# Performance work log

Hardware: AMD Instinct MI355X
Metric: run time of the kernel (lower is better)

Reference implementation:

```python
import jax, jax.numpy as jnp
import numpy as np

N_NODES = 100000
DIM = 128
N_REL = 8
N_EDGES = 640000
LAMDA = 1  # indexes into [x, z1, z2]


def setup_inputs() -> dict:
    key = jax.random.key(0)
    ks = jax.random.split(key, 6)
    x = jax.random.normal(ks[0], (N_NODES, DIM), dtype=jnp.float32)
    edge_index = jax.random.randint(ks[1], (2, N_EDGES), 0, N_NODES, dtype=jnp.int32)
    edge_type = jax.random.randint(ks[2], (N_EDGES,), 0, N_REL, dtype=jnp.int32)
    edge_weight = jax.random.uniform(ks[3], (N_EDGES,), dtype=jnp.float32)
    # xavier_uniform for [R, in, out] weight stacks (fan_in=DIM, fan_out=DIM)
    limit = float(np.sqrt(6.0 / (DIM + DIM)))
    W1 = jax.random.uniform(ks[4], (N_REL, DIM, DIM), jnp.float32, -limit, limit)
    W2 = jax.random.uniform(ks[5], (N_REL, DIM, DIM), jnp.float32, -limit, limit)
    b1 = jnp.zeros((DIM,), jnp.float32)
    b2 = jnp.zeros((DIM,), jnp.float32)
    return {"x": x, "edge_index": edge_index, "edge_type": edge_type,
            "edge_weight": edge_weight, "W1": W1, "b1": b1, "W2": W2, "b2": b2}


def _ecge_conv(x, W, b, row, col, edge_type, coef, n_nodes):
    # Faithful to: msg_e = norm_e * w_e * (x[row_e] @ W[type_e]); out = scatter_add(msg, col) + b
    # Efficient form: transform every node by every relation once (N,R,D), then gather per edge.
    xW = jnp.einsum('ni,rio->nro', x, W)          # [N, R, D]
    msg = xW[row, edge_type] * coef[:, None]       # [E, D]
    out = jax.ops.segment_sum(msg, col, num_segments=n_nodes)
    return out + b


def reference(x, edge_index, edge_type, edge_weight, W1, b1, W2, b2):
    n_nodes = x.shape[0]
    row, col = edge_index[0], edge_index[1]
    # symmetric degree normalization based on destination (col) degree
    deg = jax.ops.segment_sum(jnp.ones_like(edge_weight), col, num_segments=n_nodes)
    deg_inv_sqrt = jnp.where(deg > 0, deg ** -0.5, 0.0)
    norm = deg_inv_sqrt[row] * deg_inv_sqrt[col]
    coef = norm * edge_weight

    z1 = jax.nn.relu(_ecge_conv(x, W1, b1, row, col, edge_type, coef, n_nodes))
    # F.dropout with training=False (eval mode) is identity
    z2 = _ecge_conv(z1, W2, b2, row, col, edge_type, coef, n_nodes)

    z_star = (x + z1 + z2) / 4.0
    temp = [x, z1, z2]
    z_sharp = temp[LAMDA]
    for i in range(LAMDA + 1, 3):
        z_sharp = z_sharp + temp[i]
    z_sharp = z_sharp / (4.0 - LAMDA)
    return (z_star, z_sharp)
```

## Files before the change

### kernel.cpp

```cpp
#include <hip/hip_runtime.h>
#include <hip/hip_bf16.h>
#include <cstdint>
#include <cstddef>

#define DIM  128
#define NREL 8
#define SCB  4096
#define CPB  16

typedef __attribute__((ext_vector_type(8))) short short8;
typedef __attribute__((ext_vector_type(4))) float f32x4;

static inline int cdiv(int a, int b){ return (a + b - 1) / b; }

__device__ inline unsigned short f2bf(float f){
    union { float f; uint32_t u; } v; v.f = f;
    uint32_t u = v.u;
    uint32_t r = (u + 0x7FFFu + ((u >> 16) & 1u)) >> 16;
    return (unsigned short)r;
}
__device__ inline uint32_t pack2(float lo, float hi){
    return (uint32_t)f2bf(lo) | ((uint32_t)f2bf(hi) << 16);
}
__device__ inline float bf2f(uint32_t lo16){
    union { uint32_t u; float f; } v; v.u = lo16 << 16; return v.f;
}
__device__ inline float asf(int u){
    union { int i; float f; } v; v.i = u; return v.f;
}

__global__ __launch_bounds__(256) void k_prep(const float4* __restrict__ x, unsigned short* __restrict__ xb, int n4,
                                              const int* __restrict__ col, const int* __restrict__ et, int E,
                                              int* __restrict__ cnt8, int nb4, int eb,
                                              const float* __restrict__ W1, const float* __restrict__ W2,
                                              unsigned short* __restrict__ wpk){
    int blk = blockIdx.x;
    if (blk < nb4){
        int i = blk * 256 + threadIdx.x;
        if (i >= n4) return;
        float4 v = x[i];
        ushort4 o; o.x = f2bf(v.x); o.y = f2bf(v.y); o.z = f2bf(v.z); o.w = f2bf(v.w);
        *(ushort4*)(xb + (size_t)i * 4) = o;
    } else if (blk < nb4 + eb){
        int e = (blk - nb4) * 256 + threadIdx.x;
        if (e < E) atomicAdd(&cnt8[col[e] * NREL + et[e]], 1);
    } else {
        int b = (blk - nb4 - eb) * 4 + (threadIdx.x >> 6);
        int lane = threadIdx.x & 63;
        int ks = b & 3, nt = (b >> 2) & 7, slot = b >> 5;
        const float* Wsrc = (slot < 8) ? (W1 + (size_t)slot * DIM * DIM)
                                       : (W2 + (size_t)(slot - 8) * DIM * DIM);
        int k0 = ks * 32 + (lane >> 4) * 8;
        int n  = nt * 16 + (lane & 15);
        unsigned short o[8];
        #pragma unroll
        for (int j = 0; j < 8; ++j) o[j] = f2bf(Wsrc[(size_t)(k0 + j) * DIM + n]);
        unsigned short* dst = wpk + ((size_t)b * 64 + lane) * 8;
        #pragma unroll
        for (int j = 0; j < 8; ++j) dst[j] = o[j];
    }
}

__global__ __launch_bounds__(256) void k_colsum(const int* __restrict__ cnt8, int N, int* __restrict__ colCnt){
    int c = blockIdx.x * 256 + threadIdx.x;
    if (c >= N) return;
    int s = 0;
    #pragma unroll
    for (int t = 0; t < NREL; ++t) s += cnt8[c * NREL + t];
    colCnt[c] = s;
}

__global__ __launch_bounds__(256) void k_scan1(const int* __restrict__ cnt, int M, int* __restrict__ bsum){
    int t = threadIdx.x;
    int base = blockIdx.x * SCB + t * 16;
    int s = 0;
    #pragma unroll
    for (int k = 0; k < 16; ++k){
        int i = base + k;
        if (i < M) s += cnt[i];
    }
    #pragma unroll
    for (int o = 1; o < 64; o <<= 1) s += __shfl_xor(s, o);
    __shared__ int wsum[4];
    if ((t & 63) == 0) wsum[t >> 6] = s;
    __syncthreads();
    if (t == 0) bsum[blockIdx.x] = wsum[0] + wsum[1] + wsum[2] + wsum[3];
}

__global__ void k_scan2(int* __restrict__ bsum, int NBS, int* __restrict__ total){
    if (threadIdx.x == 0){
        int a = 0;
        for (int i = 0; i < NBS; ++i){ int v = bsum[i]; bsum[i] = a; a += v; }
        *total = a;
    }
}

__global__ __launch_bounds__(256) void k_scan3(const int* __restrict__ cnt, int M,
                                               const int* __restrict__ bsum, const int* __restrict__ total,
                                               int* __restrict__ startArr, int* __restrict__ pos){
    int t = threadIdx.x;
    int base = blockIdx.x * SCB + t * 16;
    int vals[16];
    int s = 0;
    #pragma unroll
    for (int k = 0; k < 16; ++k){
        int i = base + k;
        vals[k] = (i < M) ? cnt[i] : 0;
        s += vals[k];
    }
    int lane = t & 63, w = t >> 6;
    int v = s;
    #pragma unroll
    for (int o = 1; o < 64; o <<= 1){
        int u = __shfl_up(v, o);
        if (lane >= o) v += u;
    }
    __shared__ int wsum[4];
    if (lane == 63) wsum[w] = v;
    __syncthreads();
    int excl = v - s + bsum[blockIdx.x];
    for (int i = 0; i < w; ++i) excl += wsum[i];
    #pragma unroll
    for (int k = 0; k < 16; ++k){
        int i = base + k;
        if (i < M){ startArr[i] = excl; pos[i] = excl; excl += vals[k]; }
    }
    if (blockIdx.x == 0 && t == 0) startArr[M] = *total;
}

__global__ __launch_bounds__(256) void k_place(const int* __restrict__ row, const int* __restrict__ col,
                                               const int* __restrict__ et, const float* __restrict__ ew,
                                               const int* __restrict__ colCnt,
                                               int E, int* __restrict__ pos8, int2* __restrict__ pkm){
    int e = blockIdx.x * 256 + threadIdx.x;
    if (e >= E) return;
    int r = row[e], c = col[e], t = et[e];
    int dr = colCnt[r], dc = colCnt[c];
    float a = dr > 0 ? rsqrtf((float)dr) : 0.f;
    float b = dc > 0 ? rsqrtf((float)dc) : 0.f;
    float cf = a * b * ew[e];
    int p = atomicAdd(&pos8[c * NREL + t], 1);
    union { float f; int i; } cv; cv.f = cf;
    pkm[p] = make_int2(((c & (CPB - 1)) << 24) | (r << 3) | t, cv.i);
}

template<int MODE>
__global__ __launch_bounds__(512, 8) void k_fused(const unsigned short* __restrict__ xbin,
                                                  const unsigned short* __restrict__ wpk,
                                                  const int* __restrict__ cs8,
                                                  const int2* __restrict__ pkm,
                                                  const float* __restrict__ bias,
                                                  unsigned short* __restrict__ zb,
                                                  const unsigned short* __restrict__ xb2,
                                                  const unsigned short* __restrict__ z1b2,
                                                  float* __restrict__ outS,
                                                  float* __restrict__ outH,
                                                  int N, int wslot){
    __shared__ unsigned short s[CPB * 1024];
    int tid = threadIdx.x;
    int wid = tid >> 6, lane = tid & 63;
    int c0 = blockIdx.x * CPB;

    #pragma unroll
    for (int k = 0; k < 16; ++k) ((uint32_t*)s)[tid + 512 * k] = 0u;
    __syncthreads();

#define FLUSH() *(uint32_t*)((char*)s + flushByte) = pack2(a0, a1)
#define PROC(rt, cf, u) do{                                                       \
        int fk_ = (rt) & 0xFF000007;                                              \
        if (fk_ != fkPrev){                                                       \
            if (fkPrev >= 0) FLUSH();                                             \
            fkPrev = fk_;                                                         \
            int cl_ = ((unsigned)(rt)) >> 24; int t_ = (rt) & 7;                  \
            flushByte = cl_ * 2048 + (((t_ << 8) | (lane << 2)) ^ ((cl_ & 7) << 4)); \
            a0 = 0.f; a1 = 0.f;                                                   \
        }                                                                         \
        a0 = fmaf(cf, bf2f((u) & 0xFFFFu), a0);                                   \
        a1 = fmaf(cf, bf2f((u) >> 16),     a1); }while(0)
#define XROW(mx) ((const uint32_t*)(xbin + ((size_t)(((mx) >> 3) & 0x1FFFFF) << 7)))[lane]

    {
        int c = c0 + wid * 2;
        if (c < N){
            int cHi = c + 2; if (cHi > N) cHi = N;
            int e  = cs8[c * NREL];
            int eE = cs8[cHi * NREL];
            int fkPrev = -1;
            int flushByte = 0;
            float a0 = 0.f, a1 = 0.f;
            while (e < eE){
                int n = eE - e; if (n > 64) n = 64;
                int li = lane < n ? lane : n - 1;
                int2 mv = pkm[e + li];
                int j = 0;
                for (; j + 8 <= n; j += 8){
                    int rt[8]; float cf[8]; uint32_t u[8];
                    #pragma unroll
                    for (int k = 0; k < 8; ++k){
                        rt[k] = __builtin_amdgcn_readlane(mv.x, j + k);
                        cf[k] = asf(__builtin_amdgcn_readlane(mv.y, j + k));
                    }
                    #pragma unroll
                    for (int k = 0; k < 8; ++k) u[k] = XROW(rt[k]);
                    #pragma unroll
                    for (int k = 0; k < 8; ++k) PROC(rt[k], cf[k], u[k]);
                }
                for (; j < n; ++j){
                    int rt = __builtin_amdgcn_readlane(mv.x, j);
                    float cf = asf(__builtin_amdgcn_readlane(mv.y, j));
                    uint32_t u = XROW(rt);
                    PROC(rt, cf, u);
                }
                e += n;
            }
            if (fkPrev >= 0) FLUSH();
        }
    }
#undef PROC
#undef FLUSH
#undef XROW
    __syncthreads();

    int nt = wid;
    f32x4 acc = (f32x4){0,0,0,0};

    int al = lane & 15, ak2 = (lane >> 4) * 16;
    int swz = (al & 7) << 4;
    const char* rowA = (const char*)s + al * 2048;

    const short8* bbase = (const short8*)wpk + (size_t)wslot * 2048 + lane;

    #pragma unroll 4
    for (int ksg = 0; ksg < 32; ++ksg){
        int off = (ksg * 64 + ak2) ^ swz;
        short8 A = *(const short8*)(rowA + off);
        int t = ksg >> 2, ksl = ksg & 3;
        short8 B = (bbase + (size_t)t * 2048)[(nt * 4 + ksl) * 64];
        acc = __builtin_amdgcn_mfma_f32_16x16x32_bf16(A, B, acc, 0, 0, 0);
    }
    __syncthreads();

    float* ot = (float*)s;
    int crb = (lane >> 4) * 4, dcl = lane & 15;
    {
        int d = nt * 16 + dcl;
        float bv = bias[d];
        #pragma unroll
        for (int r = 0; r < 4; ++r){
            int mrow = crb + r;
            float v = acc[r] + bv;
            if (MODE == 0) v = fmaxf(v, 0.f);
            ot[mrow * DIM + d] = v;
        }
    }
    __syncthreads();

    if (MODE == 0){
        if (tid < 256){
            int rowi = tid >> 4, seg = tid & 15;
            int c = c0 + rowi;
            if (c < N){
                const float* src = ot + rowi * DIM + seg * 8;
                uint4 vv;
                vv.x = pack2(src[0], src[1]);
                vv.y = pack2(src[2], src[3]);
                vv.z = pack2(src[4], src[5]);
                vv.w = pack2(src[6], src[7]);
                *(uint4*)(zb + ((size_t)c << 7) + seg * 8) = vv;
            }
        }
    } else {
        int rowi = tid >> 5, q = tid & 31;
        int c = c0 + rowi;
        if (c < N){
            int d0 = q * 4;
            size_t o = ((size_t)c << 7) + d0;
            ushort4 xv4 = *(const ushort4*)(xb2 + o);
            ushort4 zv4 = *(const ushort4*)(z1b2 + o);
            const float* src = ot + rowi * DIM + d0;
            f32x4 S, H;
            {
                float xv = bf2f(xv4.x), z1 = bf2f(zv4.x), v = src[0];
                S.x = (xv + z1 + v) * 0.25f; H.x = (z1 + v) * (1.0f / 3.0f);
            }
            {
                float xv = bf2f(xv4.y), z1 = bf2f(zv4.y), v = src[1];
                S.y = (xv + z1 + v) * 0.25f; H.y = (z1 + v) * (1.0f / 3.0f);
            }
            {
                float xv = bf2f(xv4.z), z1 = bf2f(zv4.z), v = src[2];
                S.z = (xv + z1 + v) * 0.25f; H.z = (z1 + v) * (1.0f / 3.0f);
            }
            {
                float xv = bf2f(xv4.w), z1 = bf2f(zv4.w), v = src[3];
                S.w = (xv + z1 + v) * 0.25f; H.w = (z1 + v) * (1.0f / 3.0f);
            }
            __builtin_nontemporal_store(S, (f32x4*)(outS + o));
            __builtin_nontemporal_store(H, (f32x4*)(outH + o));
        }
    }
}

extern "C" void kernel_launch(void* const* d_in, const int* in_sizes, int n_in,
                              void* d_out, int out_size, void* d_ws, size_t ws_size,
                              hipStream_t stream) {
    const float* x  = (const float*)d_in[0];
    const int*   ei = (const int*)d_in[1];
    const int*   et = (const int*)d_in[2];
    const float* ew = (const float*)d_in[3];
    const float* W1 = (const float*)d_in[4];
    const float* b1 = (const float*)d_in[5];
    const float* W2 = (const float*)d_in[6];
    const float* b2 = (const float*)d_in[7];

    int E = in_sizes[2];
    int N = in_sizes[0] / DIM;
    const int* row = ei;
    const int* col = ei + E;

    float* out = (float*)d_out;
    int ND  = N * DIM;
    int ND4 = ND / 4;
    float* zS = out;
    float* zH = out + ND;

    int M8   = N * NREL;
    int NBS8 = cdiv(M8, SCB);

    char* wsb = (char*)d_ws;
    size_t off = 0;
    auto take = [&](size_t bytes) -> char* {
        char* p = wsb + off;
        off = (off + bytes + 255) & ~(size_t)255;
        return p;
    };
    int*            cnt8     = (int*)           take((size_t)M8 * 4);
    int*            start8   = (int*)           take(((size_t)M8 + 1) * 4);
    int*            pos8     = (int*)           take((size_t)M8 * 4);
    int*            colCnt   = (int*)           take((size_t)N * 4);
    int*            bsum     = (int*)           take(((size_t)NBS8 + 1) * 4);
    int2*           pkm      = (int2*)          take((size_t)E * 8);
    unsigned short* wpk      = (unsigned short*)take((size_t)16 * 2048 * 8 * 2);
    unsigned short* xb       = (unsigned short*)take((size_t)ND * 2);
    unsigned short* z1b      = (unsigned short*)take((size_t)ND * 2);
    int* total = bsum + NBS8;
    (void)n_in; (void)out_size; (void)ws_size;

    hipMemsetAsync(cnt8, 0, (size_t)M8 * 4, stream);

    int eb  = cdiv(E, 256);
    int nb4 = cdiv(ND4, 256);
    int nb  = cdiv(N, 256);
    k_prep  <<<nb4 + eb + 128, 256, 0, stream>>>((const float4*)x, xb, ND4, col, et, E, cnt8, nb4, eb, W1, W2, wpk);
    k_colsum<<<nb, 256, 0, stream>>>(cnt8, N, colCnt);
    k_scan1 <<<NBS8, 256, 0, stream>>>(cnt8, M8, bsum);
    k_scan2 <<<1, 64, 0, stream>>>(bsum, NBS8, total);
    k_scan3 <<<NBS8, 256, 0, stream>>>(cnt8, M8, bsum, total, start8, pos8);
    k_place <<<eb, 256, 0, stream>>>(row, col, et, ew, colCnt, E, pos8, pkm);

    int fb = cdiv(N, CPB);
    k_fused<0><<<fb, 512, 0, stream>>>(xb, wpk, start8, pkm, b1, z1b, nullptr, nullptr, nullptr, nullptr, N, 0);
    k_fused<1><<<fb, 512, 0, stream>>>(z1b, wpk, start8, pkm, b2, nullptr, xb, z1b, zS, zH, N, 8);
}
```

Before: 276.7 us.

## Double nodes per block and split-K MFMA with 2x2 register tiles

Doubles the nodes handled per fused block from 16 to 32, so each wave aggregates 4 destination nodes. The dense transform now splits the 8 relations across two wave halves (split-K). Each wave computes a 2x2 grid of 16x16 MFMA tiles so every A and B fragment is reused twice, and the two partial sums are added during the epilogue. The serial single-thread block-sum scan is replaced by a wave-level shuffle scan. The cost is doubled LDS per block and a lower occupancy hint.

```diff
diff --git a/kernel.cpp b/kernel.cpp
--- a/kernel.cpp
+++ b/kernel.cpp
@@ -6,7 +6,7 @@
 #define DIM  128
 #define NREL 8
 #define SCB  4096
-#define CPB  16
+#define CPB  32
 
 typedef __attribute__((ext_vector_type(8))) short short8;
 typedef __attribute__((ext_vector_type(4))) float f32x4;
@@ -88,11 +88,17 @@
 }
 
 __global__ void k_scan2(int* __restrict__ bsum, int NBS, int* __restrict__ total){
-    if (threadIdx.x == 0){
-        int a = 0;
-        for (int i = 0; i < NBS; ++i){ int v = bsum[i]; bsum[i] = a; a += v; }
-        *total = a;
-    }
+    int lane = threadIdx.x & 63;
+    int v[8]; int s = 0; int base = lane * 8;
+    #pragma unroll
+    for (int k = 0; k < 8; ++k){ int i = base + k; v[k] = (i < NBS) ? bsum[i] : 0; s += v[k]; }
+    int inc = s;
+    #pragma unroll
+    for (int o = 1; o < 64; o <<= 1){ int u = __shfl_up(inc, o); if (lane >= o) inc += u; }
+    int excl = inc - s;
+    #pragma unroll
+    for (int k = 0; k < 8; ++k){ int i = base + k; if (i < NBS) bsum[i] = excl; excl += v[k]; }
+    if (lane == 63) *total = inc;
 }
 
 __global__ __launch_bounds__(256) void k_scan3(const int* __restrict__ cnt, int M,
@@ -145,7 +151,7 @@
 }
 
 template<int MODE>
-__global__ __launch_bounds__(512, 8) void k_fused(const unsigned short* __restrict__ xbin,
+__global__ __launch_bounds__(512, 4) void k_fused(const unsigned short* __restrict__ xbin,
                                                   const unsigned short* __restrict__ wpk,
                                                   const int* __restrict__ cs8,
                                                   const int2* __restrict__ pkm,
@@ -161,8 +167,9 @@
     int wid = tid >> 6, lane = tid & 63;
     int c0 = blockIdx.x * CPB;
 
-    #pragma unroll
-    for (int k = 0; k < 16; ++k) ((uint32_t*)s)[tid + 512 * k] = 0u;
+    uint4 z4 = {0u, 0u, 0u, 0u};
+    #pragma unroll
+    for (int k = 0; k < 8; ++k) ((uint4*)s)[tid + 512 * k] = z4;
     __syncthreads();
 
 #define FLUSH() *(uint32_t*)((char*)s + flushByte) = pack2(a0, a1)
@@ -180,9 +187,9 @@
 #define XROW(mx) ((const uint32_t*)(xbin + ((size_t)(((mx) >> 3) & 0x1FFFFF) << 7)))[lane]
 
     {
-        int c = c0 + wid * 2;
+        int c = c0 + wid * 4;
         if (c < N){
-            int cHi = c + 2; if (cHi > N) cHi = N;
+            int cHi = c + 4; if (cHi > N) cHi = N;
             int e  = cs8[c * NREL];
             int eE = cs8[cHi * NREL];
             int fkPrev = -1;
@@ -221,82 +228,90 @@
 #undef XROW
     __syncthreads();
 
-    int nt = wid;
-    f32x4 acc = (f32x4){0,0,0,0};
+    int kh = wid >> 2, np = wid & 3;
+    f32x4 acc00 = {0,0,0,0}, acc01 = {0,0,0,0}, acc10 = {0,0,0,0}, acc11 = {0,0,0,0};
 
     int al = lane & 15, ak2 = (lane >> 4) * 16;
     int swz = (al & 7) << 4;
-    const char* rowA = (const char*)s + al * 2048;
-
-    const short8* bbase = (const short8*)wpk + (size_t)wslot * 2048 + lane;
+    const char* rowA0 = (const char*)s + al * 2048;
+    const char* rowA1 = rowA0 + 16 * 2048;
+
+    const short8* bb = (const short8*)wpk + (size_t)(wslot + kh * 4) * 2048 + lane;
+    const short8* b0 = bb + np * 512;
+    const short8* b1 = b0 + 256;
 
     #pragma unroll 4
-    for (int ksg = 0; ksg < 32; ++ksg){
-        int off = (ksg * 64 + ak2) ^ swz;
-        short8 A = *(const short8*)(rowA + off);
-        int t = ksg >> 2, ksl = ksg & 3;
-        short8 B = (bbase + (size_t)t * 2048)[(nt * 4 + ksl) * 64];
-        acc = __builtin_amdgcn_mfma_f32_16x16x32_bf16(A, B, acc, 0, 0, 0);
+    for (int ksg = 0; ksg < 16; ++ksg){
+        int off = (((kh * 16 + ksg) * 64) + ak2) ^ swz;
+        short8 A0 = *(const short8*)(rowA0 + off);
+        short8 A1 = *(const short8*)(rowA1 + off);
+        int bidx = (ksg >> 2) * 2048 + (ksg & 3) * 64;
+        short8 B0 = b0[bidx];
+        short8 B1 = b1[bidx];
+        acc00 = __builtin_amdgcn_mfma_f32_16x16x32_bf16(A0, B0, acc00, 0, 0, 0);
+        acc01 = __builtin_amdgcn_mfma_f32_16x16x32_bf16(A0, B1, acc01, 0, 0, 0);
+        acc10 = __builtin_amdgcn_mfma_f32_16x16x32_bf16(A1, B0, acc10, 0, 0, 0);
+        acc11 = __builtin_amdgcn_mfma_f32_16x16x32_bf16(A1, B1, acc11, 0, 0, 0);
     }
     __syncthreads();
 
     float* ot = (float*)s;
-    int crb = (lane >> 4) * 4, dcl = lane & 15;
     {
-        int d = nt * 16 + dcl;
-        float bv = bias[d];
+        int crb = (lane >> 4) * 4, dcl = lane & 15;
+        int d0 = np * 32 + dcl;
+        float* base0 = ot + kh * 4096 + crb * 128;
         #pragma unroll
         for (int r = 0; r < 4; ++r){
-            int mrow = crb + r;
-            float v = acc[r] + bv;
-            if (MODE == 0) v = fmaxf(v, 0.f);
-            ot[mrow * DIM + d] = v;
+            base0[r * 128 + d0]               = acc00[r];
+            base0[r * 128 + d0 + 16]          = acc01[r];
+            base0[(16 * 128) + r * 128 + d0]      = acc10[r];
+            base0[(16 * 128) + r * 128 + d0 + 16] = acc11[r];
         }
     }
     __syncthreads();
 
-    if (MODE == 0){
-        if (tid < 256){
-            int rowi = tid >> 4, seg = tid & 15;
-            int c = c0 + rowi;
-            if (c < N){
-                const float* src = ot + rowi * DIM + seg * 8;
-                uint4 vv;
-                vv.x = pack2(src[0], src[1]);
-                vv.y = pack2(src[2], src[3]);
-                vv.z = pack2(src[4], src[5]);
-                vv.w = pack2(src[6], src[7]);
-                *(uint4*)(zb + ((size_t)c << 7) + seg * 8) = vv;
-            }
-        }
-    } else {
-        int rowi = tid >> 5, q = tid & 31;
+    {
+        int rowi = tid >> 4, seg = tid & 15;
         int c = c0 + rowi;
         if (c < N){
-            int d0 = q * 4;
-            size_t o = ((size_t)c << 7) + d0;
-            ushort4 xv4 = *(const ushort4*)(xb2 + o);
-            ushort4 zv4 = *(const ushort4*)(z1b2 + o);
-            const float* src = ot + rowi * DIM + d0;
-            f32x4 S, H;
-            {
-                float xv = bf2f(xv4.x), z1 = bf2f(zv4.x), v = src[0];
-                S.x = (xv + z1 + v) * 0.25f; H.x = (z1 + v) * (1.0f / 3.0f);
+            int d0 = seg * 8;
+            const float* s0 = ot + rowi * DIM + d0;
+            const float* s1 = s0 + 4096;
+            float v[8];
+            #pragma unroll
+            for (int j = 0; j < 8; ++j) v[j] = s0[j] + s1[j] + bias[d0 + j];
+            if (MODE == 0){
+                #pragma unroll
+                for (int j = 0; j < 8; ++j) v[j] = fmaxf(v[j], 0.f);
+                uint4 vv;
+                vv.x = pack2(v[0], v[1]);
+                vv.y = pack2(v[2], v[3]);
+                vv.z = pack2(v[4], v[5]);
+                vv.w = pack2(v[6], v[7]);
+                *(uint4*)(zb + ((size_t)c << 7) + d0) = vv;
+            } else {
+                size_t o = ((size_t)c << 7) + d0;
+                uint4 xu = *(const uint4*)(xb2 + o);
+                uint4 zu = *(const uint4*)(z1b2 + o);
+                uint32_t xw[4] = {xu.x, xu.y, xu.z, xu.w};
+                uint32_t zw[4] = {zu.x, zu.y, zu.z, zu.w};
+                float S[8], H[8];
+                #pragma unroll
+                for (int j = 0; j < 4; ++j){
+                    float x0 = bf2f(xw[j] & 0xFFFFu), x1 = bf2f(xw[j] >> 16);
+                    float z0 = bf2f(zw[j] & 0xFFFFu), z1 = bf2f(zw[j] >> 16);
+                    S[2*j]   = (x0 + z0 + v[2*j])   * 0.25f;
+                    S[2*j+1] = (x1 + z1 + v[2*j+1]) * 0.25f;
+                    H[2*j]   = (z0 + v[2*j])   * (1.0f / 3.0f);
+                    H[2*j+1] = (z1 + v[2*j+1]) * (1.0f / 3.0f);
+                }
+                f32x4 S0 = {S[0], S[1], S[2], S[3]}, S1 = {S[4], S[5], S[6], S[7]};
+                f32x4 H0 = {H[0], H[1], H[2], H[3]}, H1 = {H[4], H[5], H[6], H[7]};
+                __builtin_nontemporal_store(S0, (f32x4*)(outS + o));
+                __builtin_nontemporal_store(S1, (f32x4*)(outS + o + 4));
+                __builtin_nontemporal_store(H0, (f32x4*)(outH + o));
+                __builtin_nontemporal_store(H1, (f32x4*)(outH + o + 4));
             }
-            {
-                float xv = bf2f(xv4.y), z1 = bf2f(zv4.y), v = src[1];
-                S.y = (xv + z1 + v) * 0.25f; H.y = (z1 + v) * (1.0f / 3.0f);
-            }
-            {
-                float xv = bf2f(xv4.z), z1 = bf2f(zv4.z), v = src[2];
-                S.z = (xv + z1 + v) * 0.25f; H.z = (z1 + v) * (1.0f / 3.0f);
-            }
-            {
-                float xv = bf2f(xv4.w), z1 = bf2f(zv4.w), v = src[3];
-                S.w = (xv + z1 + v) * 0.25f; H.w = (z1 + v) * (1.0f / 3.0f);
-            }
-            __builtin_nontemporal_store(S, (f32x4*)(outS + o));
-            __builtin_nontemporal_store(H, (f32x4*)(outH + o));
         }
     }
 }
```

Measured after the change: 269.4 us. -2.6%, faster.
